# Kernel tuning notes

Hardware: AMD Instinct MI355X
Metric: run time of the kernel (lower is better)

## Reference

```python
import jax, jax.numpy as jnp
import numpy as np

N = 20000      # nodes
E = 100000     # edges
B = 128        # graphs in batch
F_IN = 14      # node feature dim
DIM = 64       # hidden dim
E_FEAT = 4     # edge feature dim
MLP_H = 128    # edge MLP hidden


def setup_inputs() -> dict:
    key = jax.random.key(0)
    ks = jax.random.split(key, 26)

    def rn(k, shape, fan_in):
        return jax.random.normal(k, shape, jnp.float32) / np.sqrt(fan_in)

    d = {}
    d['x'] = jax.random.normal(ks[0], (N, F_IN), jnp.float32)
    d['edge_attr'] = jax.random.uniform(ks[1], (E, E_FEAT), jnp.float32)
    d['edge_index'] = jax.random.randint(ks[2], (2, E), 0, N)
    d['batch'] = jnp.sort(jax.random.randint(ks[3], (N,), 0, B))
    # lin0
    d['lin0_w'] = rn(ks[4], (F_IN, DIM), F_IN)
    d['lin0_b'] = jnp.zeros((DIM,), jnp.float32)
    # edge MLP: Linear(4,128) -> ReLU -> Linear(128, dim*dim)
    d['mlp_w1'] = rn(ks[5], (E_FEAT, MLP_H), E_FEAT)
    d['mlp_b1'] = jnp.zeros((MLP_H,), jnp.float32)
    d['mlp_w2'] = rn(ks[6], (MLP_H, DIM * DIM), MLP_H) * 0.1
    d['mlp_b2'] = jnp.zeros((DIM * DIM,), jnp.float32)
    # NNConv root weight + bias
    d['conv_root'] = rn(ks[7], (DIM, DIM), DIM)
    d['conv_bias'] = jnp.zeros((DIM,), jnp.float32)
    # GRU (input dim DIM, hidden DIM), torch gate order r,z,n
    d['gru_wi'] = rn(ks[8], (DIM, 3 * DIM), DIM)
    d['gru_wh'] = rn(ks[9], (DIM, 3 * DIM), DIM)
    d['gru_bi'] = jnp.zeros((3 * DIM,), jnp.float32)
    d['gru_bh'] = jnp.zeros((3 * DIM,), jnp.float32)
    # Set2Set LSTM (input 2*DIM, hidden DIM), torch gate order i,f,g,o
    d['lstm_wi'] = rn(ks[10], (2 * DIM, 4 * DIM), 2 * DIM)
    d['lstm_wh'] = rn(ks[11], (DIM, 4 * DIM), DIM)
    d['lstm_bi'] = jnp.zeros((4 * DIM,), jnp.float32)
    d['lstm_bh'] = jnp.zeros((4 * DIM,), jnp.float32)
    # output head
    d['lin1_w'] = rn(ks[12], (2 * DIM, DIM), 2 * DIM)
    d['lin1_b'] = jnp.zeros((DIM,), jnp.float32)
    d['lin2_w'] = rn(ks[13], (DIM, 1), DIM)
    d['lin2_b'] = jnp.zeros((1,), jnp.float32)
    return d


def _forward(x, edge_attr, edge_index, batch,
             lin0_w, lin0_b, mlp_w1, mlp_b1, mlp_w2, mlp_b2,
             conv_root, conv_bias,
             gru_wi, gru_wh, gru_bi, gru_bh,
             lstm_wi, lstm_wh, lstm_bi, lstm_bh,
             lin1_w, lin1_b, lin2_w, lin2_b):
    src, dst = edge_index[0], edge_index[1]

    out = jax.nn.relu(x @ lin0_w + lin0_b)            # [N, DIM]
    h = out                                            # GRU hidden

    # per-edge weight matrices from edge MLP (shared across the 3 steps)
    ew = jax.nn.relu(edge_attr @ mlp_w1 + mlp_b1) @ mlp_w2 + mlp_b2
    ew = ew.reshape(E, DIM, DIM)                       # [E, DIM, DIM]
    # incoming-edge counts for scatter-mean
    cnt = jax.ops.segment_sum(jnp.ones((E,), jnp.float32), dst, num_segments=N)
    cnt = jnp.maximum(cnt, 1.0)[:, None]

    for _ in range(3):
        msg = jnp.einsum('ei,eio->eo', out[src], ew)   # gather + per-edge matmul
        agg = jax.ops.segment_sum(msg, dst, num_segments=N) / cnt
        m = jax.nn.relu(agg + out @ conv_root + conv_bias)
        # GRU cell (torch gate order: r, z, n)
        gi = m @ gru_wi + gru_bi
        gh = h @ gru_wh + gru_bh
        r = jax.nn.sigmoid(gi[:, :DIM] + gh[:, :DIM])
        z = jax.nn.sigmoid(gi[:, DIM:2 * DIM] + gh[:, DIM:2 * DIM])
        n = jnp.tanh(gi[:, 2 * DIM:] + r * gh[:, 2 * DIM:])
        h = (1.0 - z) * n + z * h
        out = h

    # Set2Set pooling, 3 processing steps
    q_star = jnp.zeros((B, 2 * DIM), jnp.float32)
    hl = jnp.zeros((B, DIM), jnp.float32)
    cl = jnp.zeros((B, DIM), jnp.float32)
    for _ in range(3):
        gates = q_star @ lstm_wi + hl @ lstm_wh + lstm_bi + lstm_bh  # [B, 4*DIM]
        i = jax.nn.sigmoid(gates[:, :DIM])
        f = jax.nn.sigmoid(gates[:, DIM:2 * DIM])
        g = jnp.tanh(gates[:, 2 * DIM:3 * DIM])
        o = jax.nn.sigmoid(gates[:, 3 * DIM:])
        cl = f * cl + i * g
        hl = o * jnp.tanh(cl)
        q = hl                                         # [B, DIM]
        e = jnp.sum(out * q[batch], axis=-1)           # [N]
        emax = jax.ops.segment_max(e, batch, num_segments=B)
        emax = jnp.where(jnp.isfinite(emax), emax, 0.0)
        a = jnp.exp(e - emax[batch])
        asum = jax.ops.segment_sum(a, batch, num_segments=B)
        a = a / jnp.maximum(asum, 1e-16)[batch]
        r_vec = jax.ops.segment_sum(a[:, None] * out, batch, num_segments=B)
        q_star = jnp.concatenate([q, r_vec], axis=-1)  # [B, 2*DIM]

    y = jax.nn.relu(q_star @ lin1_w + lin1_b) @ lin2_w + lin2_b
    return y.reshape(-1)                               # [B]


def reference(x, edge_attr, edge_index, batch,
              lin0_w, lin0_b, mlp_w1, mlp_b1, mlp_w2, mlp_b2,
              conv_root, conv_bias,
              gru_wi, gru_wh, gru_bi, gru_bh,
              lstm_wi, lstm_wh, lstm_bi, lstm_bh,
              lin1_w, lin1_b, lin2_w, lin2_b):
    return _forward(x, edge_attr, edge_index, batch,
                    lin0_w, lin0_b, mlp_w1, mlp_b1, mlp_w2, mlp_b2,
                    conv_root, conv_bias,
                    gru_wi, gru_wh, gru_bi, gru_bh,
                    lstm_wi, lstm_wh, lstm_bi, lstm_bh,
                    lin1_w, lin1_b, lin2_w, lin2_b)
```

## Files before the change

kernel.cpp:

```cpp
#include <hip/hip_runtime.h>
#include <math.h>

#define N_ 20000
#define E_ 100000
#define B_ 128
#define F_IN_ 14
#define DIM_ 64
#define E_FEAT_ 4
#define MLP_H_ 128
#define EWC_ 4096
#define PC_ 8192
#define PC2_ 8256

#define LIN0_BLKS 5000
#define DEG_BLKS 391
#define PREPB_BLKS 2064

typedef __attribute__((ext_vector_type(4))) float f32x4;
typedef __attribute__((ext_vector_type(8))) _Float16 halfx8;

__global__ __launch_bounds__(256) void setup_a(
        const float* __restrict__ x, const float* __restrict__ lw,
        const float* __restrict__ lb, float* __restrict__ out,
        const int* __restrict__ src, const int* __restrict__ dst,
        float* __restrict__ cnt, int* __restrict__ cnt_src,
        const int* __restrict__ batch, int* __restrict__ off_b,
        const float* __restrict__ w2, const float* __restrict__ b2,
        _Float16* __restrict__ Bf) {
    int b = blockIdx.x;
    int t = threadIdx.x;
    if (b < LIN0_BLKS) {
        int idx = b * 256 + t;
        int n = idx >> 6, d = idx & 63;
        float acc = lb[d];
#pragma unroll
        for (int f = 0; f < F_IN_; ++f) acc = fmaf(x[n * F_IN_ + f], lw[f * DIM_ + d], acc);
        out[idx] = acc > 0.f ? acc : 0.f;
    } else if (b < LIN0_BLKS + DEG_BLKS) {
        int e = (b - LIN0_BLKS) * 256 + t;
        if (e < E_) {
            atomicAdd(&cnt[dst[e]], 1.0f);
            atomicAdd(&cnt_src[src[e]], 1);
        }
        if (b == LIN0_BLKS && t <= B_) {
            int bb = t;
            int lo = 0, hi = N_;
            while (lo < hi) {
                int mid = (lo + hi) >> 1;
                if (batch[mid] < bb) lo = mid + 1; else hi = mid;
            }
            off_b[bb] = lo;
        }
    } else {
        int idx = (b - LIN0_BLKS - DEG_BLKS) * 256 + t;
        if (idx >= PC2_ * 64) return;
        int c16 = idx >> 10;
        int r   = idx & 1023;
        int ks  = r >> 9;
        int q   = (r >> 7) & 3;
        int lr  = (r >> 3) & 15;
        int j   = r & 7;
        int c = c16 * 16 + lr;
        int i = ks * 32 + q * 8 + j;
        float v;
        if (c < PC_) {
            int o = c >> 7, k = c & 127;
            v = w2[(size_t)k * EWC_ + i * 64 + o];
        } else {
            int o = c - PC_;
            v = b2[i * 64 + o];
        }
        Bf[idx] = (_Float16)v;
    }
}

__global__ void scan_src(const int* __restrict__ cnt_src, int* __restrict__ src_off) {
    __shared__ int part[256];
    __shared__ int off[257];
    int t = threadIdx.x;
    const int per = (N_ + 255) / 256;
    int base = t * per;
    int s = 0;
    for (int i = 0; i < per; ++i) { int b = base + i; if (b < N_) s += cnt_src[b]; }
    part[t] = s;
    __syncthreads();
    if (t == 0) {
        int a = 0;
        for (int i = 0; i < 256; ++i) { off[i] = a; a += part[i]; }
        off[256] = a;
    }
    __syncthreads();
    int run = off[t];
    for (int i = 0; i < per; ++i) {
        int b = base + i;
        if (b < N_) { src_off[b] = run; run += cnt_src[b]; }
    }
    if (t == 0) src_off[N_] = off[256];
}

__global__ __launch_bounds__(256) void scatter_mlp1(
        const int* __restrict__ src, const int* __restrict__ dst,
        int* __restrict__ cur, const int* __restrict__ src_off,
        const float* __restrict__ ea, const float* __restrict__ w1,
        const float* __restrict__ b1, int* __restrict__ dsts,
        _Float16* __restrict__ h1s) {
    __shared__ float w1s[E_FEAT_ * MLP_H_];
    __shared__ float b1s[MLP_H_];
    int t = threadIdx.x;
    if (t < MLP_H_) b1s[t] = b1[t];
    for (int i = t; i < E_FEAT_ * MLP_H_; i += 256) w1s[i] = w1[i];
    __syncthreads();
    int e = blockIdx.x * 256 + t;
    if (e >= E_) return;
    int s = src[e];
    int p = src_off[s] + atomicAdd(&cur[s], 1);
    dsts[p] = dst[e];
    float a0 = ea[e * 4 + 0], a1 = ea[e * 4 + 1];
    float a2 = ea[e * 4 + 2], a3 = ea[e * 4 + 3];
    _Float16* hrow = h1s + (size_t)p * 128;
#pragma unroll
    for (int k8 = 0; k8 < 16; ++k8) {
        halfx8 v;
#pragma unroll
        for (int j = 0; j < 8; ++j) {
            int k = k8 * 8 + j;
            float acc = b1s[k];
            acc = fmaf(a0, w1s[k], acc);
            acc = fmaf(a1, w1s[128 + k], acc);
            acc = fmaf(a2, w1s[256 + k], acc);
            acc = fmaf(a3, w1s[384 + k], acc);
            v[j] = (_Float16)(acc > 0.f ? acc : 0.f);
        }
        *(halfx8*)&hrow[k8 * 8] = v;
    }
}

__global__ __launch_bounds__(512, 4) void fused_msg(
        const float* __restrict__ out, const _Float16* __restrict__ Bf,
        const _Float16* __restrict__ h1s,
        const int* __restrict__ dsts, const int* __restrict__ src_off,
        float* __restrict__ agg) {
    __shared__ _Float16 Plds[16 * 2048];
    const int tid = threadIdx.x;
    const int lane = tid & 63;
    const int w = __builtin_amdgcn_readfirstlane(tid >> 6);
    const int lrow = lane & 15, quad = lane >> 4;
    const int nb0 = blockIdx.x * 16;

    halfx8 aG[2];
    {
        const float* orow = out + (size_t)(nb0 + lrow) * 64 + quad * 8;
#pragma unroll
        for (int ks = 0; ks < 2; ++ks) {
            float4 v0 = *(const float4*)(orow + ks * 32);
            float4 v1 = *(const float4*)(orow + ks * 32 + 4);
            aG[ks][0] = (_Float16)v0.x; aG[ks][1] = (_Float16)v0.y;
            aG[ks][2] = (_Float16)v0.z; aG[ks][3] = (_Float16)v0.w;
            aG[ks][4] = (_Float16)v1.x; aG[ks][5] = (_Float16)v1.y;
            aG[ks][6] = (_Float16)v1.z; aG[ks][7] = (_Float16)v1.w;
        }
    }

    f32x4 qf[4];
#pragma unroll
    for (int f = 0; f < 4; ++f) {
        const _Float16* bc = &Bf[(size_t)(512 + f) * 1024 + quad * 128 + lrow * 8];
        halfx8 bq0 = *(const halfx8*)bc;
        halfx8 bq1 = *(const halfx8*)(bc + 512);
        f32x4 z = (f32x4){0.f, 0.f, 0.f, 0.f};
        z = __builtin_amdgcn_mfma_f32_16x16x32_f16(aG[0], bq0, z, 0, 0, 0);
        z = __builtin_amdgcn_mfma_f32_16x16x32_f16(aG[1], bq1, z, 0, 0, 0);
        qf[f] = z;
    }

    const int n0g = nb0 + 2 * w;
    const int beg0 = src_off[n0g];
    const int end0 = src_off[n0g + 1];
    const int end1 = src_off[n0g + 2];

#pragma unroll
    for (int p = 0; p < 4; ++p) {
        if (p) __syncthreads();

#pragma unroll 8
        for (int nf = 0; nf < 16; ++nf) {
            int cl = w * 256 + nf * 16 + lrow;
            size_t tb = (size_t)(p * 128 + w * 16 + nf) * 1024 + quad * 128 + lrow * 8;
            halfx8 b0 = *(const halfx8*)&Bf[tb];
            halfx8 b1 = *(const halfx8*)&Bf[tb + 512];
            f32x4 acc = (f32x4){0.f, 0.f, 0.f, 0.f};
            acc = __builtin_amdgcn_mfma_f32_16x16x32_f16(aG[0], b0, acc, 0, 0, 0);
            acc = __builtin_amdgcn_mfma_f32_16x16x32_f16(aG[1], b1, acc, 0, 0, 0);
            int o = cl >> 7, k = cl & 127;
            int kz = k ^ (quad << 5) ^ ((o & 7) << 3);
            int base = o * 2048 + kz;
#pragma unroll
            for (int rr = 0; rr < 4; ++rr)
                Plds[base + (quad * 4 + rr) * 128] = (_Float16)acc[rr];
        }
        __syncthreads();

        int o0 = p * 16;
#pragma unroll
        for (int nn = 0; nn < 2; ++nn) {
            int nl = 2 * w + nn;
            int beg = nn ? end0 : beg0;
            int endv = nn ? end1 : end0;
            if (beg == endv) continue;
            int srcl = ((nl >> 2) << 4) | lrow;
            int rsel = nl & 3;
            float qel = rsel == 0 ? qf[p][0] : rsel == 1 ? qf[p][1]
                      : rsel == 2 ? qf[p][2] : qf[p][3];
            float qv = __shfl(qel, srcl, 64);
            halfx8 bf[4];
#pragma unroll
            for (int ks = 0; ks < 4; ++ks) {
                int kk = (ks * 32 + quad * 8) ^ ((nl >> 2) << 5) ^ ((lrow & 7) << 3);
                bf[ks] = *(const halfx8*)&Plds[lrow * 2048 + nl * 128 + kk];
            }
            for (int g = beg; g < endv; g += 16) {
                int gcnt = endv - g; if (gcnt > 16) gcnt = 16;
                int ei = lrow < gcnt ? lrow : gcnt - 1;
                int gi = g + ei;
                int dv = dsts[gi];
                halfx8 af[4];
#pragma unroll
                for (int ks = 0; ks < 4; ++ks)
                    af[ks] = *(const halfx8*)&h1s[(size_t)gi * 128 + ks * 32 + quad * 8];
                f32x4 acc = (f32x4){0.f, 0.f, 0.f, 0.f};
#pragma unroll
                for (int ks = 0; ks < 4; ++ks)
                    acc = __builtin_amdgcn_mfma_f32_16x16x32_f16(
                        af[ks], bf[ks], acc, 0, 0, 0);
#pragma unroll
                for (int rr = 0; rr < 4; ++rr) {
                    int j = quad * 4 + rr;
                    int d = __shfl(dv, j, 64);
                    if (j < gcnt) {
                        atomicAdd(&agg[(size_t)d * 64 + o0 + lrow], acc[rr] + qv);
                    }
                }
            }
        }
    }
}

__global__ __launch_bounds__(256) void gru_kernel(float* __restrict__ out,
                                                  float* __restrict__ agg,
                                                  const float* __restrict__ cnt,
                                                  const float* __restrict__ root,
                                                  const float* __restrict__ cbias,
                                                  const float* __restrict__ wi,
                                                  const float* __restrict__ wh,
                                                  const float* __restrict__ bi,
                                                  const float* __restrict__ bh) {
    __shared__ float root_s[64 * 64];
    __shared__ float h_s[32 * 64];
    __shared__ float m_s[32 * 64];
    int tid = threadIdx.x;
    int lane = tid & 63;
    int wv = __builtin_amdgcn_readfirstlane(tid >> 6);
    int nb = blockIdx.x * 32;
#pragma unroll
    for (int it = 0; it < 4; ++it) {
        int i = it * 1024 + tid * 4;
        *(float4*)&root_s[i] = *(const float4*)&root[i];
    }
#pragma unroll
    for (int it = 0; it < 2; ++it) {
        int i = it * 1024 + tid * 4;
        *(float4*)&h_s[i] = *(const float4*)&out[(size_t)nb * 64 + i];
    }
    __syncthreads();

    int nbase = nb + wv * 8;
    float a[8];
#pragma unroll
    for (int j = 0; j < 8; ++j) {
        int n = nbase + j;
        float c = cnt[n]; c = c > 1.f ? c : 1.f;
        a[j] = agg[(size_t)n * 64 + lane] / c + cbias[lane];
        agg[(size_t)n * 64 + lane] = 0.f;
    }
    for (int i = 0; i < 64; ++i) {
        float rv = root_s[i * 64 + lane];
#pragma unroll
        for (int j = 0; j < 8; ++j)
            a[j] = fmaf(h_s[(wv * 8 + j) * 64 + i], rv, a[j]);
    }
#pragma unroll
    for (int j = 0; j < 8; ++j) {
        float m = a[j] > 0.f ? a[j] : 0.f;
        m_s[(wv * 8 + j) * 64 + lane] = m;
    }
    __syncthreads();

    float gir[8], giz[8], gin[8], ghr[8], ghz[8], ghn[8];
    float bi0 = bi[lane], bi1 = bi[64 + lane], bi2 = bi[128 + lane];
    float bh0 = bh[lane], bh1 = bh[64 + lane], bh2 = bh[128 + lane];
#pragma unroll
    for (int j = 0; j < 8; ++j) {
        gir[j] = bi0; giz[j] = bi1; gin[j] = bi2;
        ghr[j] = bh0; ghz[j] = bh1; ghn[j] = bh2;
    }
    for (int i = 0; i < 64; ++i) {
        float w0 = wi[i * 192 + lane];
        float w1 = wi[i * 192 + 64 + lane];
        float w2v = wi[i * 192 + 128 + lane];
        float u0 = wh[i * 192 + lane];
        float u1 = wh[i * 192 + 64 + lane];
        float u2 = wh[i * 192 + 128 + lane];
#pragma unroll
        for (int j = 0; j < 8; ++j) {
            float mi = m_s[(wv * 8 + j) * 64 + i];
            float hi = h_s[(wv * 8 + j) * 64 + i];
            gir[j] = fmaf(mi, w0, gir[j]);
            giz[j] = fmaf(mi, w1, giz[j]);
            gin[j] = fmaf(mi, w2v, gin[j]);
            ghr[j] = fmaf(hi, u0, ghr[j]);
            ghz[j] = fmaf(hi, u1, ghz[j]);
            ghn[j] = fmaf(hi, u2, ghn[j]);
        }
    }
#pragma unroll
    for (int j = 0; j < 8; ++j) {
        int n = nbase + j;
        float rg = 1.f / (1.f + expf(-(gir[j] + ghr[j])));
        float zg = 1.f / (1.f + expf(-(giz[j] + ghz[j])));
        float ng = tanhf(gin[j] + rg * ghn[j]);
        float h = h_s[(wv * 8 + j) * 64 + lane];
        out[(size_t)n * 64 + lane] = (1.f - zg) * ng + zg * h;
    }
}

__global__ __launch_bounds__(256) void lstm_all_kernel(
        const float* __restrict__ out, const int* __restrict__ off_b,
        float* __restrict__ e_ws,
        const float* __restrict__ wi, const float* __restrict__ wh,
        const float* __restrict__ bi, const float* __restrict__ bh,
        const float* __restrict__ hw1, const float* __restrict__ hb1,
        const float* __restrict__ hw2, const float* __restrict__ hb2,
        float* __restrict__ y) {
    int b = blockIdx.x;
    int t = threadIdx.x;
    __shared__ float qs[128], hs[64], cs[64], g[256];
    __shared__ float q[64];
    __shared__ float red[256], racc[256], sasum[4];

    if (t < 128) qs[t] = 0.f;
    if (t < 64) { hs[t] = 0.f; cs[t] = 0.f; }
    __syncthreads();

    int start = off_b[b], end = off_b[b + 1];

    for (int s = 0; s < 3; ++s) {
        {
            float acc = bi[t] + bh[t];
#pragma unroll 8
            for (int i = 0; i < 128; ++i) acc = fmaf(qs[i], wi[i * 256 + t], acc);
#pragma unroll 8
            for (int i = 0; i < 64; ++i) acc = fmaf(hs[i], wh[i * 256 + t], acc);
            g[t] = acc;
        }
        __syncthreads();
        if (t < 64) {
            float ig = 1.f / (1.f + expf(-g[t]));
            float fg = 1.f / (1.f + expf(-g[64 + t]));
            float gg = tanhf(g[128 + t]);
            float og = 1.f / (1.f + expf(-g[192 + t]));
            float c = fg * cs[t] + ig * gg;
            cs[t] = c;
            float h = og * tanhf(c);
            hs[t] = h;
            q[t] = h;
        }
        __syncthreads();

        float lmax = -1e30f;
        for (int n = start + t; n < end; n += 256) {
            float acc = 0.f;
#pragma unroll 16
            for (int d2 = 0; d2 < 64; ++d2) acc = fmaf(out[n * 64 + d2], q[d2], acc);
            e_ws[n] = acc;
            lmax = fmaxf(lmax, acc);
        }
        red[t] = lmax;
        __syncthreads();
        for (int s2 = 128; s2 > 0; s2 >>= 1) {
            if (t < s2) red[t] = fmaxf(red[t], red[t + s2]);
            __syncthreads();
        }
        float emax = red[0];
        int w = t >> 6, d = t & 63;
        float rl = 0.f, lasum = 0.f;
        for (int n = start + w; n < end; n += 4) {
            float a = expf(e_ws[n] - emax);
            rl = fmaf(a, out[n * 64 + d], rl);
            if (d == 0) lasum += a;
        }
        racc[t] = rl;
        if (d == 0) sasum[w] = lasum;
        __syncthreads();
        if (t < 64) {
            float r = racc[t] + racc[64 + t] + racc[128 + t] + racc[192 + t];
            float as = sasum[0] + sasum[1] + sasum[2] + sasum[3];
            as = fmaxf(as, 1e-16f);
            qs[t] = q[t];
            qs[64 + t] = r / as;
        }
        __syncthreads();
    }

    if (t < 64) {
        float acc = hb1[t];
#pragma unroll 8
        for (int i = 0; i < 128; ++i) acc = fmaf(qs[i], hw1[i * 64 + t], acc);
        acc = acc > 0.f ? acc : 0.f;
        float p = acc * hw2[t];
        for (int off = 32; off > 0; off >>= 1) p += __shfl_down(p, off, 64);
        if (t == 0) y[b] = p + hb2[0];
    }
}

extern "C" void kernel_launch(void* const* d_in, const int* in_sizes, int n_in,
                              void* d_out, int out_size, void* d_ws, size_t ws_size,
                              hipStream_t stream) {
    (void)in_sizes; (void)n_in; (void)out_size; (void)ws_size;
    const float* x        = (const float*)d_in[0];
    const float* ea       = (const float*)d_in[1];
    const int*   eidx     = (const int*)d_in[2];
    const int*   batch    = (const int*)d_in[3];
    const float* lin0_w   = (const float*)d_in[4];
    const float* lin0_b   = (const float*)d_in[5];
    const float* mlp_w1   = (const float*)d_in[6];
    const float* mlp_b1   = (const float*)d_in[7];
    const float* mlp_w2   = (const float*)d_in[8];
    const float* mlp_b2   = (const float*)d_in[9];
    const float* conv_root= (const float*)d_in[10];
    const float* conv_bias= (const float*)d_in[11];
    const float* gru_wi   = (const float*)d_in[12];
    const float* gru_wh   = (const float*)d_in[13];
    const float* gru_bi   = (const float*)d_in[14];
    const float* gru_bh   = (const float*)d_in[15];
    const float* lstm_wi  = (const float*)d_in[16];
    const float* lstm_wh  = (const float*)d_in[17];
    const float* lstm_bi  = (const float*)d_in[18];
    const float* lstm_bh  = (const float*)d_in[19];
    const float* lin1_w   = (const float*)d_in[20];
    const float* lin1_b   = (const float*)d_in[21];
    const float* lin2_w   = (const float*)d_in[22];
    const float* lin2_b   = (const float*)d_in[23];
    float* y = (float*)d_out;

    const int* src = eidx;
    const int* dst = eidx + E_;

    char* w = (char*)d_ws;
    auto carve = [&](size_t bytes) {
        char* p = w;
        w += (bytes + 255) & ~(size_t)255;
        return p;
    };
    float* out_buf = (float*)carve((size_t)N_ * DIM_ * 4);
    float* e_ws    = (float*)carve((size_t)N_ * 4);
    int*   off_b   = (int*)carve((size_t)(B_ + 1) * 4);
    _Float16* h1s  = (_Float16*)carve((size_t)E_ * MLP_H_ * 2);
    _Float16* Bf   = (_Float16*)carve((size_t)PC2_ * 64 * 2);
    int*   src_off = (int*)carve((size_t)(N_ + 1) * 4);
    int*   dsts    = (int*)carve((size_t)E_ * 4);
    char*  zero0   = w;
    float* agg     = (float*)carve((size_t)N_ * DIM_ * 4);
    float* cnt     = (float*)carve((size_t)N_ * 4);
    int*   cnt_src = (int*)carve((size_t)N_ * 4);
    int*   cur     = (int*)carve((size_t)N_ * 4);
    size_t zbytes  = (size_t)(w - zero0);

    hipMemsetAsync(zero0, 0, zbytes, stream);

    setup_a<<<LIN0_BLKS + DEG_BLKS + PREPB_BLKS, 256, 0, stream>>>(
        x, lin0_w, lin0_b, out_buf, src, dst, cnt, cnt_src, batch, off_b,
        mlp_w2, mlp_b2, Bf);
    scan_src<<<1, 256, 0, stream>>>(cnt_src, src_off);
    scatter_mlp1<<<(E_ + 255) / 256, 256, 0, stream>>>(src, dst, cur, src_off,
                                                       ea, mlp_w1, mlp_b1,
                                                       dsts, h1s);

    for (int step = 0; step < 3; ++step) {
        fused_msg<<<N_ / 16, 512, 0, stream>>>(out_buf, Bf, h1s, dsts,
                                               src_off, agg);
        gru_kernel<<<N_ / 32, 256, 0, stream>>>(out_buf, agg, cnt, conv_root,
                                                conv_bias, gru_wi, gru_wh,
                                                gru_bi, gru_bh);
    }

    lstm_all_kernel<<<B_, 256, 0, stream>>>(out_buf, off_b, e_ws,
                                            lstm_wi, lstm_wh, lstm_bi, lstm_bh,
                                            lin1_w, lin1_b, lin2_w, lin2_b, y);
}
```

Measured before the change: 574.8 us.

## Process 32 source nodes per fused_msg block to reuse weight tile loads

Each fused_msg block now handles two 16-node groups instead of one, so each Bf weight fragment loaded from global memory feeds two MFMA chains. The per-node projected weights are staged in an LDS buffer twice as large, and each wave walks edges for four nodes instead of two. This halves the global reads of Bf per node, at the cost of doubled LDS use, lower occupancy (launch bounds reduced to 2 blocks per SIMD) and half as many blocks.

Result: slower. 625.0 us (+8.7%).

```diff
diff --git a/kernel.cpp b/kernel.cpp
--- a/kernel.cpp
+++ b/kernel.cpp
@@ -135,48 +135,59 @@
     }
 }
 
-__global__ __launch_bounds__(512, 4) void fused_msg(
+__global__ __launch_bounds__(512, 2) void fused_msg(
         const float* __restrict__ out, const _Float16* __restrict__ Bf,
         const _Float16* __restrict__ h1s,
         const int* __restrict__ dsts, const int* __restrict__ src_off,
         float* __restrict__ agg) {
-    __shared__ _Float16 Plds[16 * 2048];
+    __shared__ _Float16 Plds[16 * 4096];
     const int tid = threadIdx.x;
     const int lane = tid & 63;
     const int w = __builtin_amdgcn_readfirstlane(tid >> 6);
     const int lrow = lane & 15, quad = lane >> 4;
-    const int nb0 = blockIdx.x * 16;
-
-    halfx8 aG[2];
+    const int nb0 = blockIdx.x * 32;
+
+    halfx8 aA[2], aB[2];
     {
-        const float* orow = out + (size_t)(nb0 + lrow) * 64 + quad * 8;
+        const float* orowA = out + (size_t)(nb0 + lrow) * 64 + quad * 8;
+        const float* orowB = out + (size_t)(nb0 + 16 + lrow) * 64 + quad * 8;
 #pragma unroll
         for (int ks = 0; ks < 2; ++ks) {
-            float4 v0 = *(const float4*)(orow + ks * 32);
-            float4 v1 = *(const float4*)(orow + ks * 32 + 4);
-            aG[ks][0] = (_Float16)v0.x; aG[ks][1] = (_Float16)v0.y;
-            aG[ks][2] = (_Float16)v0.z; aG[ks][3] = (_Float16)v0.w;
-            aG[ks][4] = (_Float16)v1.x; aG[ks][5] = (_Float16)v1.y;
-            aG[ks][6] = (_Float16)v1.z; aG[ks][7] = (_Float16)v1.w;
-        }
-    }
-
-    f32x4 qf[4];
+            float4 v0 = *(const float4*)(orowA + ks * 32);
+            float4 v1 = *(const float4*)(orowA + ks * 32 + 4);
+            aA[ks][0] = (_Float16)v0.x; aA[ks][1] = (_Float16)v0.y;
+            aA[ks][2] = (_Float16)v0.z; aA[ks][3] = (_Float16)v0.w;
+            aA[ks][4] = (_Float16)v1.x; aA[ks][5] = (_Float16)v1.y;
+            aA[ks][6] = (_Float16)v1.z; aA[ks][7] = (_Float16)v1.w;
+            float4 u0 = *(const float4*)(orowB + ks * 32);
+            float4 u1 = *(const float4*)(orowB + ks * 32 + 4);
+            aB[ks][0] = (_Float16)u0.x; aB[ks][1] = (_Float16)u0.y;
+            aB[ks][2] = (_Float16)u0.z; aB[ks][3] = (_Float16)u0.w;
+            aB[ks][4] = (_Float16)u1.x; aB[ks][5] = (_Float16)u1.y;
+            aB[ks][6] = (_Float16)u1.z; aB[ks][7] = (_Float16)u1.w;
+        }
+    }
+
+    f32x4 qfA[4], qfB[4];
 #pragma unroll
     for (int f = 0; f < 4; ++f) {
         const _Float16* bc = &Bf[(size_t)(512 + f) * 1024 + quad * 128 + lrow * 8];
         halfx8 bq0 = *(const halfx8*)bc;
         halfx8 bq1 = *(const halfx8*)(bc + 512);
         f32x4 z = (f32x4){0.f, 0.f, 0.f, 0.f};
-        z = __builtin_amdgcn_mfma_f32_16x16x32_f16(aG[0], bq0, z, 0, 0, 0);
-        z = __builtin_amdgcn_mfma_f32_16x16x32_f16(aG[1], bq1, z, 0, 0, 0);
-        qf[f] = z;
-    }
-
-    const int n0g = nb0 + 2 * w;
-    const int beg0 = src_off[n0g];
-    const int end0 = src_off[n0g + 1];
-    const int end1 = src_off[n0g + 2];
+        z = __builtin_amdgcn_mfma_f32_16x16x32_f16(aA[0], bq0, z, 0, 0, 0);
+        z = __builtin_amdgcn_mfma_f32_16x16x32_f16(aA[1], bq1, z, 0, 0, 0);
+        qfA[f] = z;
+        f32x4 z2 = (f32x4){0.f, 0.f, 0.f, 0.f};
+        z2 = __builtin_amdgcn_mfma_f32_16x16x32_f16(aB[0], bq0, z2, 0, 0, 0);
+        z2 = __builtin_amdgcn_mfma_f32_16x16x32_f16(aB[1], bq1, z2, 0, 0, 0);
+        qfB[f] = z2;
+    }
+
+    const int nA = nb0 + 2 * w;
+    const int nB = nb0 + 16 + 2 * w;
+    const int begA0 = src_off[nA], endA0 = src_off[nA + 1], endA1 = src_off[nA + 2];
+    const int begB0 = src_off[nB], endB0 = src_off[nB + 1], endB1 = src_off[nB + 2];
 
 #pragma unroll
     for (int p = 0; p < 4; ++p) {
@@ -188,35 +199,45 @@
             size_t tb = (size_t)(p * 128 + w * 16 + nf) * 1024 + quad * 128 + lrow * 8;
             halfx8 b0 = *(const halfx8*)&Bf[tb];
             halfx8 b1 = *(const halfx8*)&Bf[tb + 512];
-            f32x4 acc = (f32x4){0.f, 0.f, 0.f, 0.f};
-            acc = __builtin_amdgcn_mfma_f32_16x16x32_f16(aG[0], b0, acc, 0, 0, 0);
-            acc = __builtin_amdgcn_mfma_f32_16x16x32_f16(aG[1], b1, acc, 0, 0, 0);
+            f32x4 accA = (f32x4){0.f, 0.f, 0.f, 0.f};
+            f32x4 accB = (f32x4){0.f, 0.f, 0.f, 0.f};
+            accA = __builtin_amdgcn_mfma_f32_16x16x32_f16(aA[0], b0, accA, 0, 0, 0);
+            accA = __builtin_amdgcn_mfma_f32_16x16x32_f16(aA[1], b1, accA, 0, 0, 0);
+            accB = __builtin_amdgcn_mfma_f32_16x16x32_f16(aB[0], b0, accB, 0, 0, 0);
+            accB = __builtin_amdgcn_mfma_f32_16x16x32_f16(aB[1], b1, accB, 0, 0, 0);
             int o = cl >> 7, k = cl & 127;
             int kz = k ^ (quad << 5) ^ ((o & 7) << 3);
-            int base = o * 2048 + kz;
-#pragma unroll
-            for (int rr = 0; rr < 4; ++rr)
-                Plds[base + (quad * 4 + rr) * 128] = (_Float16)acc[rr];
+            int base = o * 4096 + kz;
+#pragma unroll
+            for (int rr = 0; rr < 4; ++rr) {
+                Plds[base + (quad * 4 + rr) * 128] = (_Float16)accA[rr];
+                Plds[base + (16 + quad * 4 + rr) * 128] = (_Float16)accB[rr];
+            }
         }
         __syncthreads();
 
         int o0 = p * 16;
 #pragma unroll
-        for (int nn = 0; nn < 2; ++nn) {
-            int nl = 2 * w + nn;
-            int beg = nn ? end0 : beg0;
-            int endv = nn ? end1 : end0;
+        for (int nn = 0; nn < 4; ++nn) {
+            int nl15 = 2 * w + (nn & 1);
+            int nl = ((nn >> 1) << 4) | nl15;
+            int beg  = (nn == 0) ? begA0 : (nn == 1) ? endA0
+                     : (nn == 2) ? begB0 : endB0;
+            int endv = (nn == 0) ? endA0 : (nn == 1) ? endA1
+                     : (nn == 2) ? endB0 : endB1;
             if (beg == endv) continue;
-            int srcl = ((nl >> 2) << 4) | lrow;
-            int rsel = nl & 3;
-            float qel = rsel == 0 ? qf[p][0] : rsel == 1 ? qf[p][1]
-                      : rsel == 2 ? qf[p][2] : qf[p][3];
+            f32x4 qq = (nn >> 1) ? qfB[p] : qfA[p];
+            int rsel = nl15 & 3;
+            float qel = rsel == 0 ? qq[0] : rsel == 1 ? qq[1]
+                      : rsel == 2 ? qq[2] : qq[3];
+            int srcl = ((nl15 >> 2) << 4) | lrow;
             float qv = __shfl(qel, srcl, 64);
             halfx8 bf[4];
 #pragma unroll
             for (int ks = 0; ks < 4; ++ks) {
-                int kk = (ks * 32 + quad * 8) ^ ((nl >> 2) << 5) ^ ((lrow & 7) << 3);
-                bf[ks] = *(const halfx8*)&Plds[lrow * 2048 + nl * 128 + kk];
+                int kk = (ks * 32 + quad * 8) ^ (((nl >> 2) & 3) << 5)
+                       ^ ((lrow & 7) << 3);
+                bf[ks] = *(const halfx8*)&Plds[lrow * 4096 + nl * 128 + kk];
             }
             for (int g = beg; g < endv; g += 16) {
                 int gcnt = endv - g; if (gcnt > 16) gcnt = 16;
@@ -486,7 +507,7 @@
                                                        dsts, h1s);
 
     for (int step = 0; step < 3; ++step) {
-        fused_msg<<<N_ / 16, 512, 0, stream>>>(out_buf, Bf, h1s, dsts,
+        fused_msg<<<N_ / 32, 512, 0, stream>>>(out_buf, Bf, h1s, dsts,
                                                src_off, agg);
         gru_kernel<<<N_ / 32, 256, 0, stream>>>(out_buf, agg, cnt, conv_root,
                                                 conv_bias, gru_wi, gru_wh,
```
